# Kernel optimization log

Measured on AMD Instinct MI355X. Metric: run time of the kernel, lower is better.

## Reference

```python
import jax, jax.numpy as jnp
import numpy as np

B = 2
IM_H, IM_W = 240, 320
ENV_ROW, ENV_COL = 120, 160
ENV_H, ENV_W = 8, 16
GRID = 8
NGRIDS = 6 * GRID * GRID  # 384
BASIS = [(3, 2, 0), (7, 6, 4), (4, 5, 0), (6, 2, 5), (7, 6, 3), (7, 3, 4)]
# extra_transform_matrix @ extra_transform_matrix_LightNet, applied to row vectors
M12 = jnp.asarray(np.array([[0., 0., 1.], [0., -1., 0.], [1., 0., 0.]], np.float32)
                  @ np.array([[1., 0., 0.], [0., -1., 0.], [0., 0., -1.]], np.float32))


def _normalize(v, axis):
    return v / jnp.maximum(jnp.linalg.norm(v, axis=axis, keepdims=True), 1e-12)


def _inv3x3(A):
    # closed-form adjugate inverse of batched 3x3 (replaces torch.inverse)
    a, b, c = A[..., 0, 0], A[..., 0, 1], A[..., 0, 2]
    d, e, f = A[..., 1, 0], A[..., 1, 1], A[..., 1, 2]
    g, h, i = A[..., 2, 0], A[..., 2, 1], A[..., 2, 2]
    c00 = e * i - f * h; c01 = f * g - d * i; c02 = d * h - e * g
    c10 = c * h - b * i; c11 = a * i - c * g; c12 = b * g - a * h
    c20 = b * f - c * e; c21 = c * d - a * f; c22 = a * e - b * d
    det = a * c00 + b * c01 + c * c02
    inv = jnp.stack([jnp.stack([c00, c10, c20], -1),
                     jnp.stack([c01, c11, c21], -1),
                     jnp.stack([c02, c12, c22], -1)], -2)
    return inv / det[..., None, None]


def _camera_frame(normalPred):
    # renderingLayer.forwardEnv(if_normal_only=True): pool normal to env res,
    # renormalize, build per-pixel (camx, camy, normal) frame with up=[0,1,0]
    r = IM_H // ENV_ROW
    n = normalPred.reshape(normalPred.shape[0], 3, ENV_ROW, r, ENV_COL, r).mean(axis=(3, 5))
    n = n / jnp.sqrt(jnp.clip(jnp.sum(n * n, axis=1, keepdims=True), 1e-6, 1.0))
    up = jnp.array([0., 1., 0.], n.dtype).reshape(1, 3, 1, 1)
    camy = _normalize(up - jnp.sum(up * n, axis=1, keepdims=True) * n, 1)
    camx = -_normalize(jnp.cross(camy, n, axis=1), 1)
    return camx, camy, n


def _grid_centers(layout, cam_R):
    # get_grid_centers: 6 walls x GRID x GRID cell centers, transformed to LightNet frame.
    # The transform is linear with t=0, so mean-of-4-corners == center = b1*(i+.5)+b2*(j+.5)+o.
    o = jnp.stack([layout[:, t[0]] for t in BASIS], 1)                 # (B,6,3)
    b1 = (jnp.stack([layout[:, t[1]] for t in BASIS], 1) - o) / GRID
    b2 = (jnp.stack([layout[:, t[2]] for t in BASIS], 1) - o) / GRID
    ii, jj = jnp.meshgrid(jnp.arange(GRID, dtype=layout.dtype), jnp.arange(GRID, dtype=layout.dtype), indexing='ij')
    ctr = (b1[:, :, None, None, :] * (ii + 0.5)[None, None, :, :, None]
           + b2[:, :, None, None, :] * (jj + 0.5)[None, None, :, :, None]
           + o[:, :, None, None, :])                                   # (B,6,G,G,3)
    ctr = jnp.einsum('bji,bfghj->bfghi', cam_R, ctr)                   # R^T @ v
    ctr = jnp.einsum('bfghi,ij->bfghj', ctr, M12)                      # row-vec @ M1 @ M2
    return ctr.reshape(layout.shape[0], -1, 3)                         # (B, 384, 3)


def _sample_env_border(env, x, y):
    # grid_sample(align_corners=True, padding_mode='border') on the 8x16 env hemisphere.
    # With align_corners=True the normalized uv unnormalizes back to pixel coords (az, el).
    H, W = ENV_H, ENV_W
    x = jnp.clip(x, 0.0, W - 1.0); y = jnp.clip(y, 0.0, H - 1.0)
    x0f = jnp.floor(x); y0f = jnp.floor(y)
    wx = (x - x0f)[..., None]; wy = (y - y0f)[..., None]
    x0 = x0f.astype(jnp.int32); y0 = y0f.astype(jnp.int32)
    x1 = jnp.minimum(x0 + 1, W - 1); y1 = jnp.minimum(y0 + 1, H - 1)
    envp = jnp.transpose(env, (0, 1, 2, 4, 5, 3)).reshape(env.shape[0], ENV_ROW, ENV_COL, H * W, 3)

    def g(yy, xx):
        return jnp.take_along_axis(envp, (yy * W + xx)[..., None], axis=3)  # (B,R,C,N,3)

    return (g(y0, x0) * (1 - wy) * (1 - wx) + g(y0, x1) * (1 - wy) * wx
            + g(y1, x0) * wy * (1 - wx) + g(y1, x1) * wy * wx)


def _forward(normalPred, depthPred, envmapsPredImage, cam_K, cam_R, layout):
    f_pix = (cam_K[:, 0, 0] * (IM_W / 2.0) / cam_K[:, 0, 2])[:, None, None]
    vv, uu = jnp.meshgrid(jnp.arange(IM_H, dtype=depthPred.dtype), jnp.arange(IM_W, dtype=depthPred.dtype), indexing='ij')
    z = -depthPred
    points = jnp.stack([-(uu - IM_W / 2.0) / f_pix * z, (vv - IM_H / 2.0) / f_pix * z, z], axis=1)  # (B,3,IM_H,IM_W)

    camx, camy, nrm = _camera_frame(normalPred)      # (B,3,R,C) each
    centers = _grid_centers(layout, cam_R)           # (B,NG,3)

    r = IM_H // ENV_ROW
    pts = jnp.transpose(points[:, :, ::r, ::r], (0, 2, 3, 1))  # (B,R,C,3)
    mask = (pts[..., 2] < -0.1).astype(points.dtype)           # (B,R,C)

    A = jnp.stack([jnp.transpose(camx, (0, 2, 3, 1)),
                   jnp.transpose(camy, (0, 2, 3, 1)),
                   jnp.transpose(nrm, (0, 2, 3, 1))], axis=-1)  # (B,R,C,3,3) columns
    Ainv = _inv3x3(A + 1e-6 * jnp.eye(3, dtype=A.dtype))

    vec = centers[:, :, None, None, :] - pts[:, None]           # (B,NG,R,C,3)
    l = jnp.einsum('brcij,bnrcj->bnrci', Ainv, vec)
    l = l / jnp.linalg.norm(l, axis=-1, keepdims=True)
    cos_t = jnp.clip(l[..., 2], -1.0, 1.0)
    theta = jnp.arccos(cos_t)
    sin_t = jnp.sin(theta)
    phi = jnp.arctan2(l[..., 1] / sin_t, l[..., 0] / sin_t)
    az = (phi / (2.0 * np.pi) + 0.5) * ENV_W - 0.5              # (B,NG,R,C)
    el = theta / np.pi * 2.0 * ENV_H - 0.5

    env = jnp.transpose(envmapsPredImage, (0, 2, 3, 1, 4, 5))   # (B,R,C,3,H,W)
    sampled = _sample_env_border(env, jnp.transpose(az, (0, 2, 3, 1)), jnp.transpose(el, (0, 2, 3, 1)))  # (B,R,C,NG,3)

    acc = jnp.transpose(sampled, (0, 4, 3, 1, 2)) * mask[:, None, None] * 0.1  # (B,3,NG,R,C)
    mask_exp = mask[:, None, None]                                             # (B,1,1,R,C)
    mean = jnp.transpose(acc.sum((-1, -2)) / (mask_exp.sum((-1, -2)) + 1e-6), (0, 2, 1))  # (B,NG,3)
    return acc, mask_exp, mean


def setup_inputs() -> dict:
    key = jax.random.key(0)
    k1, k2, k3, k4, k5, k6 = jax.random.split(key, 6)
    normalPred = jax.random.normal(k1, (B, 3, IM_H, IM_W), jnp.float32)
    normalPred = normalPred / jnp.maximum(jnp.linalg.norm(normalPred, axis=1, keepdims=True), 1e-6)
    depthPred = jax.random.uniform(k2, (B, IM_H, IM_W), jnp.float32, 0.5, 5.5)
    envmapsPredImage = jax.random.uniform(k3, (B, 3, ENV_ROW, ENV_COL, ENV_H, ENV_W), jnp.float32)
    f = 250.0 + 100.0 * jax.random.uniform(k4, (B,), jnp.float32)
    z0 = jnp.zeros((B,), jnp.float32); o1 = jnp.ones((B,), jnp.float32)
    cam_K = jnp.stack([jnp.stack([f, z0, o1 * (IM_W / 2.0)], -1),
                       jnp.stack([z0, f, o1 * (IM_H / 2.0)], -1),
                       jnp.stack([z0, z0, o1], -1)], 1)
    ang = jax.random.uniform(k5, (B,), jnp.float32, -0.3, 0.3)
    ca, sa = jnp.cos(ang), jnp.sin(ang)
    cam_R = jnp.stack([jnp.stack([ca, z0, sa], -1),
                       jnp.stack([z0, o1, z0], -1),
                       jnp.stack([-sa, z0, ca], -1)], 1)
    box = jnp.asarray(np.array([[-3, -1.5, -3], [3, -1.5, -3], [3, -1.5, 3], [-3, -1.5, 3],
                                [-3, 1.5, -3], [3, 1.5, -3], [3, 1.5, 3], [-3, 1.5, 3]], np.float32))
    layout = box[None] + 0.05 * jax.random.normal(k6, (B, 8, 3), jnp.float32)
    return {"normalPred": normalPred, "depthPred": depthPred, "envmapsPredImage": envmapsPredImage,
            "cam_K": cam_K, "cam_R": cam_R, "layout": layout}


def reference(normalPred, depthPred, envmapsPredImage, cam_K, cam_R, layout):
    # returns (envmap_lightAccu, points_sampled_mask_expanded, envmap_lightAccu_mean)
    return _forward(normalPred, depthPred, envmapsPredImage, cam_K, cam_R, layout)
```

## Files before the change

kernel.cpp:

```cpp
#include <hip/hip_runtime.h>

typedef unsigned short u16;
typedef unsigned int   u32;

#define IM_H    240
#define IM_W    320
#define ENV_COL 160
#define NPIX    19200
#define NGRIDS  384
#define BATCH   2

#define ACC_SIZE (BATCH*3*NGRIDS*NPIX)
#define MASK_OFF ACC_SIZE
#define MEAN_OFF (ACC_SIZE + BATCH*NPIX)

#define NREP    8
#define WS_SUM8    0
#define WS_MSUM8   (BATCH*NREP*1152)
#define WS_ZERO_F  (WS_MSUM8 + BATCH*NREP)

#define PI_F  3.14159265358979f
#define PI_2F 1.57079632679490f

__device__ __forceinline__ u16 f2bf(float f) {
    u32 x = __float_as_uint(f);
    x += 0x7fffu + ((x >> 16) & 1u);
    return (u16)(x >> 16);
}

__device__ __forceinline__ float row16_sum(float v) {
    v += __int_as_float(__builtin_amdgcn_update_dpp(
             0, __float_as_int(v), 0x128, 0xf, 0xf, false));
    v += __int_as_float(__builtin_amdgcn_update_dpp(
             0, __float_as_int(v), 0x124, 0xf, 0xf, false));
    v += __int_as_float(__builtin_amdgcn_update_dpp(
             0, __float_as_int(v), 0x122, 0xf, 0xf, false));
    v += __int_as_float(__builtin_amdgcn_update_dpp(
             0, __float_as_int(v), 0x121, 0xf, 0xf, false));
    return v;
}

__device__ __forceinline__ float fast_acos(float x) {
    float ax = fabsf(x);
    float s  = sqrtf(fmaxf(1.0f - ax, 0.0f));
    float p  = ((-0.0187293f * ax + 0.0742610f) * ax - 0.2121144f) * ax + 1.5707288f;
    float r  = s * p;
    return (x < 0.0f) ? (PI_F - r) : r;
}

__device__ __forceinline__ float fast_atan2(float y, float x) {
    float ax = fabsf(x), ay = fabsf(y);
    float mx = fmaxf(ax, ay), mn = fminf(ax, ay);
    float t  = mn * __builtin_amdgcn_rcpf(fmaxf(mx, 1e-37f));
    float t2 = t * t;
    float p  = ((((0.0208351f * t2 - 0.0851330f) * t2 + 0.1801410f) * t2
                 - 0.3302995f) * t2 + 0.9998660f) * t;
    p = (ay > ax) ? (PI_2F - p) : p;
    p = (x < 0.0f) ? (PI_F - p) : p;
    return __builtin_copysignf(p, y);
}

__global__ __launch_bounds__(256, 4) void k_main(
        const float* __restrict__ normal,
        const float* __restrict__ depth,
        const float* __restrict__ envm,
        const float* __restrict__ camK,
        const float* __restrict__ camR,
        const float* __restrict__ layout,
        float* __restrict__ wsum8,
        float* __restrict__ msum8,
        float* __restrict__ out) {

    __shared__ __align__(16) u32   env01[128 * 32];
    __shared__               u16   env2 [128 * 32];
    __shared__ __align__(16) float cen_s[NGRIDS * 4];
    __shared__               float pgeo[32][13];
    __shared__               float psum[NGRIDS * 3];
    __shared__               float pmask;

    const int tid = threadIdx.x;
    const int bid = blockIdx.x;
    const int b   = bid / 600;
    const int pg  = bid % 600;
    const int p0  = pg * 32;

    for (int i = tid; i < NGRIDS * 3; i += 256) psum[i] = 0.0f;
    if (tid == 0) pmask = 0.0f;

    {
        const int B0[6] = {3, 7, 4, 6, 7, 7};
        const int B1[6] = {2, 6, 5, 2, 6, 3};
        const int B2[6] = {0, 4, 0, 5, 3, 4};
        for (int idx = tid; idx < NGRIDS; idx += 256) {
            int f = idx >> 6, gi = (idx >> 3) & 7, hj = idx & 7;
            int t0 = B0[f], t1 = B1[f], t2 = B2[f];
            float cw[3];
            #pragma unroll
            for (int j = 0; j < 3; ++j) {
                float o  = layout[(b * 8 + t0) * 3 + j];
                float e1 = (layout[(b * 8 + t1) * 3 + j] - o) * 0.125f;
                float e2 = (layout[(b * 8 + t2) * 3 + j] - o) * 0.125f;
                cw[j] = e1 * ((float)gi + 0.5f) + e2 * ((float)hj + 0.5f) + o;
            }
            float v0 = camR[b*9+0]*cw[0] + camR[b*9+3]*cw[1] + camR[b*9+6]*cw[2];
            float v1 = camR[b*9+1]*cw[0] + camR[b*9+4]*cw[1] + camR[b*9+7]*cw[2];
            float v2 = camR[b*9+2]*cw[0] + camR[b*9+5]*cw[1] + camR[b*9+8]*cw[2];
            cen_s[idx * 4 + 0] = v2;
            cen_s[idx * 4 + 1] = v1;
            cen_s[idx * 4 + 2] = -v0;
            cen_s[idx * 4 + 3] = 0.0f;
        }
    }

    #pragma unroll
    for (int k = 0; k < 4; ++k) {
        int ci  = tid + k * 256;
        int pix = ci & 31;
        int tq  = ci >> 5;
        size_t base = ((size_t)b * 3 * NPIX + p0 + pix) * 128 + tq * 4;
        const float4 v0 = *reinterpret_cast<const float4*>(&envm[base]);
        const float4 v1 = *reinterpret_cast<const float4*>(&envm[base + (size_t)NPIX * 128]);
        const float4 v2 = *reinterpret_cast<const float4*>(&envm[base + (size_t)2 * NPIX * 128]);
        const float a0[4] = {v0.x, v0.y, v0.z, v0.w};
        const float a1[4] = {v1.x, v1.y, v1.z, v1.w};
        const float a2[4] = {v2.x, v2.y, v2.z, v2.w};
        #pragma unroll
        for (int j = 0; j < 4; ++j) {
            int t = tq * 4 + j;
            env01[t * 32 + pix] = ((u32)f2bf(a1[j]) << 16) | (u32)f2bf(a0[j]);
            env2 [t * 32 + pix] = f2bf(a2[j]);
        }
    }

    if (tid < 32) {
        int p = p0 + tid;
        int r = p / ENV_COL, c = p % ENV_COL;
        float nv[3];
        #pragma unroll
        for (int ch = 0; ch < 3; ++ch) {
            const float* np_ = &normal[((size_t)(b * 3 + ch) * IM_H + 2 * r) * IM_W + 2 * c];
            nv[ch] = 0.25f * (np_[0] + np_[1] + np_[IM_W] + np_[IM_W + 1]);
        }
        float s2 = nv[0]*nv[0] + nv[1]*nv[1] + nv[2]*nv[2];
        s2 = fminf(fmaxf(s2, 1e-6f), 1.0f);
        float inv = 1.0f / sqrtf(s2);
        nv[0] *= inv; nv[1] *= inv; nv[2] *= inv;
        float ty0 = -nv[1]*nv[0], ty1 = 1.0f - nv[1]*nv[1], ty2 = -nv[1]*nv[2];
        float tn = fmaxf(sqrtf(ty0*ty0 + ty1*ty1 + ty2*ty2), 1e-12f);
        float cy0 = ty0/tn, cy1 = ty1/tn, cy2 = ty2/tn;
        float cr0 = cy1*nv[2] - cy2*nv[1];
        float cr1 = cy2*nv[0] - cy0*nv[2];
        float cr2 = cy0*nv[1] - cy1*nv[0];
        float cnm = fmaxf(sqrtf(cr0*cr0 + cr1*cr1 + cr2*cr2), 1e-12f);
        float cx0 = -cr0/cnm, cx1 = -cr1/cnm, cx2 = -cr2/cnm;
        float a = cx0 + 1e-6f, bb = cy0,         cc = nv[0];
        float d = cx1,         e  = cy1 + 1e-6f, f  = nv[1];
        float g2 = cx2,        h  = cy2,         i  = nv[2] + 1e-6f;
        float c00 = e*i - f*h,   c01 = f*g2 - d*i,  c02 = d*h - e*g2;
        float c10 = cc*h - bb*i, c11 = a*i - cc*g2, c12 = bb*g2 - a*h;
        float c20 = bb*f - cc*e, c21 = cc*d - a*f,  c22 = a*e - bb*d;
        float rdet = 1.0f / (a*c00 + bb*c01 + cc*c02);
        float K00 = camK[b * 9 + 0];
        float K02 = camK[b * 9 + 2];
        float fpix = K00 * (IM_W / 2.0f) / K02;
        float z = -depth[((size_t)b * IM_H + 2 * r) * IM_W + 2 * c];
        float px = -((2.0f * c) - IM_W / 2.0f) / fpix * z;
        float py =  ((2.0f * r) - IM_H / 2.0f) / fpix * z;
        float mask = (z < -0.1f) ? 1.0f : 0.0f;
        pgeo[tid][0] = px;  pgeo[tid][1] = py;  pgeo[tid][2] = z;
        pgeo[tid][3] = c00*rdet; pgeo[tid][4]  = c10*rdet; pgeo[tid][5]  = c20*rdet;
        pgeo[tid][6] = c01*rdet; pgeo[tid][7]  = c11*rdet; pgeo[tid][8]  = c21*rdet;
        pgeo[tid][9] = c02*rdet; pgeo[tid][10] = c12*rdet; pgeo[tid][11] = c22*rdet;
        pgeo[tid][12] = mask;
        out[MASK_OFF + (size_t)b * NPIX + p] = mask;
    }

    __syncthreads();

    if (tid < 32) {
        float ms = row16_sum(pgeo[tid][12]);
        if ((tid & 15) == 0) atomicAdd(&pmask, ms);
    }

    const int pix  = tid & 31;
    const int slot = tid >> 5;
    const float ptx = pgeo[pix][0], pty = pgeo[pix][1], ptz = pgeo[pix][2];
    const float A0 = pgeo[pix][3], A1 = pgeo[pix][4],  A2 = pgeo[pix][5];
    const float A3 = pgeo[pix][6], A4 = pgeo[pix][7],  A5 = pgeo[pix][8];
    const float A6 = pgeo[pix][9], A7 = pgeo[pix][10], A8 = pgeo[pix][11];
    const float mscale = pgeo[pix][12] * 0.1f;

    #pragma unroll 4
    for (int it = 0; it < 48; ++it) {
        const int n = it * 8 + slot;
        const float4 cc4 = *reinterpret_cast<const float4*>(&cen_s[n * 4]);
        const float vx = cc4.x - ptx;
        const float vy = cc4.y - pty;
        const float vz = cc4.z - ptz;
        float lx = A0 * vx + A1 * vy + A2 * vz;
        float ly = A3 * vx + A4 * vy + A5 * vz;
        float lz = A6 * vx + A7 * vy + A8 * vz;
        float rn = __builtin_amdgcn_rsqf(lx * lx + ly * ly + lz * lz);
        float ct = fminf(fmaxf(lz * rn, -1.0f), 1.0f);
        float theta = fast_acos(ct);
        float phi = fast_atan2(ly, lx);
        float az = phi * 2.54647908947032537f + 7.5f;
        float el = theta * 5.09295817894065074f - 0.5f;
        float x = fminf(fmaxf(az, 0.0f), 15.0f);
        float y = fminf(fmaxf(el, 0.0f), 7.0f);
        float x0f = floorf(x), y0f = floorf(y);
        float wx = x - x0f, wy = y - y0f;
        int ix0 = (int)x0f, iy0 = (int)y0f;
        int ix1 = min(ix0 + 1, 15), iy1 = min(iy0 + 1, 7);
        int t00 = (iy0 << 4) + ix0;
        int t01 = (iy0 << 4) + ix1;
        int t10 = (iy1 << 4) + ix0;
        int t11 = (iy1 << 4) + ix1;
        u32 c00 = env01[(t00 << 5) + pix], c01 = env01[(t01 << 5) + pix];
        u32 c10 = env01[(t10 << 5) + pix], c11 = env01[(t11 << 5) + pix];
        u32 g00 = env2 [(t00 << 5) + pix], g01 = env2 [(t01 << 5) + pix];
        u32 g10 = env2 [(t10 << 5) + pix], g11 = env2 [(t11 << 5) + pix];
        float wy1m = wy * mscale, wy0m = mscale - wy1m;
        float w00 = wy0m * (1.0f - wx), w01 = wy0m * wx;
        float w10 = wy1m * (1.0f - wx), w11 = wy1m * wx;
        float v0 = w00 * __uint_as_float(c00 << 16)
                 + w01 * __uint_as_float(c01 << 16)
                 + w10 * __uint_as_float(c10 << 16)
                 + w11 * __uint_as_float(c11 << 16);
        float v1 = w00 * __uint_as_float(c00 & 0xffff0000u)
                 + w01 * __uint_as_float(c01 & 0xffff0000u)
                 + w10 * __uint_as_float(c10 & 0xffff0000u)
                 + w11 * __uint_as_float(c11 & 0xffff0000u);
        float v2 = w00 * __uint_as_float(g00 << 16)
                 + w01 * __uint_as_float(g01 << 16)
                 + w10 * __uint_as_float(g10 << 16)
                 + w11 * __uint_as_float(g11 << 16);

        size_t obase = ((size_t)b * 3 * NGRIDS + n) * NPIX + p0 + pix;
        out[obase]                             = v0;
        out[obase + (size_t)NGRIDS * NPIX]     = v1;
        out[obase + (size_t)2 * NGRIDS * NPIX] = v2;

        float s0 = row16_sum(v0);
        float s1 = row16_sum(v1);
        float s2v = row16_sum(v2);
        if ((pix & 15) == 0) {
            atomicAdd(&psum[n * 3 + 0], s0);
            atomicAdd(&psum[n * 3 + 1], s1);
            atomicAdd(&psum[n * 3 + 2], s2v);
        }
    }

    __syncthreads();
    {
        float* wrep = &wsum8[((size_t)b * NREP + (bid & (NREP - 1))) * (NGRIDS * 3)];
        for (int i = tid; i < NGRIDS * 3; i += 256)
            atomicAdd(&wrep[i], psum[i]);
        if (tid == 0)
            atomicAdd(&msum8[b * NREP + (bid & (NREP - 1))], pmask);
    }
}

__global__ __launch_bounds__(256) void k_final(const float* __restrict__ wsum8,
                                               const float* __restrict__ msum8,
                                               float* __restrict__ out) {
    int t = blockIdx.x * 256 + threadIdx.x;
    if (t >= BATCH * NGRIDS * 3) return;
    int b = t / (NGRIDS * 3);
    int i = t % (NGRIDS * 3);
    float ms = 0.0f;
    #pragma unroll
    for (int r = 0; r < NREP; ++r) ms += msum8[b * NREP + r];
    float s = 0.0f;
    #pragma unroll
    for (int r = 0; r < NREP; ++r)
        s += wsum8[((size_t)b * NREP + r) * (NGRIDS * 3) + i];
    out[MEAN_OFF + t] = s / (ms + 1e-6f);
}

extern "C" void kernel_launch(void* const* d_in, const int* in_sizes, int n_in,
                              void* d_out, int out_size, void* d_ws, size_t ws_size,
                              hipStream_t stream) {
    const float* normal = (const float*)d_in[0];
    const float* depth  = (const float*)d_in[1];
    const float* envm   = (const float*)d_in[2];
    const float* camK   = (const float*)d_in[3];
    const float* camR   = (const float*)d_in[4];
    const float* layout = (const float*)d_in[5];
    float* out = (float*)d_out;
    float* ws  = (float*)d_ws;

    hipMemsetAsync(ws, 0, WS_ZERO_F * sizeof(float), stream);
    k_main<<<dim3(BATCH * 600), dim3(256), 0, stream>>>(normal, depth, envm, camK,
                                                        camR, layout,
                                                        ws + WS_SUM8, ws + WS_MSUM8,
                                                        out);
    k_final<<<dim3(9), dim3(256), 0, stream>>>(ws + WS_SUM8, ws + WS_MSUM8, out);
}
```

Measured before the change: 274.5 us.

## Replace atomic reductions with per-block partial sums and a two-stage final reduce

Each block now writes its half-wave partial sums of the envmap values and of the mask directly to a workspace buffer instead of doing shared-memory atomics followed by global atomics into replicated accumulators. The memset of the workspace is removed. The final kernel becomes a tree reduction over 1200 partials per output element. This removes the atomic contention and the memset launch, but adds roughly 10 MB of partial-sum writes and a strided gather read in k_final.

```diff
diff --git a/kernel.cpp b/kernel.cpp
--- a/kernel.cpp
+++ b/kernel.cpp
@@ -14,10 +14,9 @@
 #define MASK_OFF ACC_SIZE
 #define MEAN_OFF (ACC_SIZE + BATCH*NPIX)
 
-#define NREP    8
-#define WS_SUM8    0
-#define WS_MSUM8   (BATCH*NREP*1152)
-#define WS_ZERO_F  (WS_MSUM8 + BATCH*NREP)
+#define WS_WPART   0
+#define WPART_N    (BATCH*600*2*1152)
+#define WS_MPART   WPART_N
 
 #define PI_F  3.14159265358979f
 #define PI_2F 1.57079632679490f
@@ -67,25 +66,20 @@
         const float* __restrict__ camK,
         const float* __restrict__ camR,
         const float* __restrict__ layout,
-        float* __restrict__ wsum8,
-        float* __restrict__ msum8,
+        float* __restrict__ wpart,
+        float* __restrict__ mpart,
         float* __restrict__ out) {
 
     __shared__ __align__(16) u32   env01[128 * 32];
     __shared__               u16   env2 [128 * 32];
     __shared__ __align__(16) float cen_s[NGRIDS * 4];
     __shared__               float pgeo[32][13];
-    __shared__               float psum[NGRIDS * 3];
-    __shared__               float pmask;
 
     const int tid = threadIdx.x;
     const int bid = blockIdx.x;
     const int b   = bid / 600;
     const int pg  = bid % 600;
     const int p0  = pg * 32;
-
-    for (int i = tid; i < NGRIDS * 3; i += 256) psum[i] = 0.0f;
-    if (tid == 0) pmask = 0.0f;
 
     {
         const int B0[6] = {3, 7, 4, 6, 7, 7};
@@ -173,14 +167,11 @@
         pgeo[tid][9] = c02*rdet; pgeo[tid][10] = c12*rdet; pgeo[tid][11] = c22*rdet;
         pgeo[tid][12] = mask;
         out[MASK_OFF + (size_t)b * NPIX + p] = mask;
+        float ms = row16_sum(mask);
+        if ((tid & 15) == 0) mpart[bid * 2 + (tid >> 4)] = ms;
     }
 
     __syncthreads();
-
-    if (tid < 32) {
-        float ms = row16_sum(pgeo[tid][12]);
-        if ((tid & 15) == 0) atomicAdd(&pmask, ms);
-    }
 
     const int pix  = tid & 31;
     const int slot = tid >> 5;
@@ -189,6 +180,7 @@
     const float A3 = pgeo[pix][6], A4 = pgeo[pix][7],  A5 = pgeo[pix][8];
     const float A6 = pgeo[pix][9], A7 = pgeo[pix][10], A8 = pgeo[pix][11];
     const float mscale = pgeo[pix][12] * 0.1f;
+    float* const wbase = &wpart[((size_t)bid * 2 + (pix >> 4)) * 1152];
 
     #pragma unroll 4
     for (int it = 0; it < 48; ++it) {
@@ -245,37 +237,36 @@
         float s1 = row16_sum(v1);
         float s2v = row16_sum(v2);
         if ((pix & 15) == 0) {
-            atomicAdd(&psum[n * 3 + 0], s0);
-            atomicAdd(&psum[n * 3 + 1], s1);
-            atomicAdd(&psum[n * 3 + 2], s2v);
-        }
-    }
-
+            float* wp = wbase + n * 3;
+            wp[0] = s0;
+            wp[1] = s1;
+            wp[2] = s2v;
+        }
+    }
+}
+
+__global__ __launch_bounds__(256) void k_final(const float* __restrict__ wpart,
+                                               const float* __restrict__ mpart,
+                                               float* __restrict__ out) {
+    const int bid = blockIdx.x;
+    const int tid = threadIdx.x;
+    const int b   = bid / 1152;
+    const int i   = bid % 1152;
+    float s = 0.0f, ms = 0.0f;
+    for (int j = tid; j < 1200; j += 256) {
+        s  += wpart[((size_t)b * 1200 + j) * 1152 + i];
+        ms += mpart[b * 1200 + j];
+    }
+    __shared__ float r1[256], r2[256];
+    r1[tid] = s; r2[tid] = ms;
     __syncthreads();
-    {
-        float* wrep = &wsum8[((size_t)b * NREP + (bid & (NREP - 1))) * (NGRIDS * 3)];
-        for (int i = tid; i < NGRIDS * 3; i += 256)
-            atomicAdd(&wrep[i], psum[i]);
-        if (tid == 0)
-            atomicAdd(&msum8[b * NREP + (bid & (NREP - 1))], pmask);
-    }
-}
-
-__global__ __launch_bounds__(256) void k_final(const float* __restrict__ wsum8,
-                                               const float* __restrict__ msum8,
-                                               float* __restrict__ out) {
-    int t = blockIdx.x * 256 + threadIdx.x;
-    if (t >= BATCH * NGRIDS * 3) return;
-    int b = t / (NGRIDS * 3);
-    int i = t % (NGRIDS * 3);
-    float ms = 0.0f;
     #pragma unroll
-    for (int r = 0; r < NREP; ++r) ms += msum8[b * NREP + r];
-    float s = 0.0f;
-    #pragma unroll
-    for (int r = 0; r < NREP; ++r)
-        s += wsum8[((size_t)b * NREP + r) * (NGRIDS * 3) + i];
-    out[MEAN_OFF + t] = s / (ms + 1e-6f);
+    for (int m = 128; m >= 1; m >>= 1) {
+        if (tid < m) { r1[tid] += r1[tid + m]; r2[tid] += r2[tid + m]; }
+        __syncthreads();
+    }
+    if (tid == 0)
+        out[MEAN_OFF + bid] = r1[0] / (r2[0] + 1e-6f);
 }
 
 extern "C" void kernel_launch(void* const* d_in, const int* in_sizes, int n_in,
@@ -290,10 +281,10 @@
     float* out = (float*)d_out;
     float* ws  = (float*)d_ws;
 
-    hipMemsetAsync(ws, 0, WS_ZERO_F * sizeof(float), stream);
     k_main<<<dim3(BATCH * 600), dim3(256), 0, stream>>>(normal, depth, envm, camK,
                                                         camR, layout,
-                                                        ws + WS_SUM8, ws + WS_MSUM8,
+                                                        ws + WS_WPART, ws + WS_MPART,
                                                         out);
-    k_final<<<dim3(9), dim3(256), 0, stream>>>(ws + WS_SUM8, ws + WS_MSUM8, out);
-}
+    k_final<<<dim3(BATCH * 1152), dim3(256), 0, stream>>>(ws + WS_WPART,
+                                                          ws + WS_MPART, out);
+}
```

Result: slower. 295.2 us (+7.5%).

## Precompute grid centers in separate kernel and compute pixel geometry per-thread

Applied to the files above, without the earlier changes.

Moves the grid-center computation out of k_main into a tiny k_centers kernel that writes centers to workspace; k_main then reads them from global memory (L1/L2 cached) instead of shared memory. Per-pixel geometry is now computed redundantly by all 256 threads in registers rather than by 32 threads and shared via LDS. Together these free shared memory (cen_s, pgeo) and raise launch_bounds occupancy target from 4 to 5 blocks per SM. The trade-off is an extra launch, 8x redundant per-pixel geometry and normal loads, and global-memory center loads in the hot loop.

```diff
diff --git a/kernel.cpp b/kernel.cpp
--- a/kernel.cpp
+++ b/kernel.cpp
@@ -18,6 +18,7 @@
 #define WS_SUM8    0
 #define WS_MSUM8   (BATCH*NREP*1152)
 #define WS_ZERO_F  (WS_MSUM8 + BATCH*NREP)
+#define WS_CEN     WS_ZERO_F
 
 #define PI_F  3.14159265358979f
 #define PI_2F 1.57079632679490f
@@ -60,21 +61,46 @@
     return __builtin_copysignf(p, y);
 }
 
-__global__ __launch_bounds__(256, 4) void k_main(
+__global__ __launch_bounds__(256) void k_centers(const float* __restrict__ layout,
+                                                 const float* __restrict__ camR,
+                                                 float* __restrict__ cen) {
+    int t = blockIdx.x * 256 + threadIdx.x;
+    if (t >= BATCH * NGRIDS) return;
+    int b = t / NGRIDS, n = t % NGRIDS;
+    int f = n >> 6, gi = (n >> 3) & 7, hj = n & 7;
+    const int B0[6] = {3, 7, 4, 6, 7, 7};
+    const int B1[6] = {2, 6, 5, 2, 6, 3};
+    const int B2[6] = {0, 4, 0, 5, 3, 4};
+    int t0 = B0[f], t1 = B1[f], t2 = B2[f];
+    float cw[3];
+    #pragma unroll
+    for (int j = 0; j < 3; ++j) {
+        float o  = layout[(b * 8 + t0) * 3 + j];
+        float e1 = (layout[(b * 8 + t1) * 3 + j] - o) * 0.125f;
+        float e2 = (layout[(b * 8 + t2) * 3 + j] - o) * 0.125f;
+        cw[j] = e1 * ((float)gi + 0.5f) + e2 * ((float)hj + 0.5f) + o;
+    }
+    float v0 = camR[b*9+0]*cw[0] + camR[b*9+3]*cw[1] + camR[b*9+6]*cw[2];
+    float v1 = camR[b*9+1]*cw[0] + camR[b*9+4]*cw[1] + camR[b*9+7]*cw[2];
+    float v2 = camR[b*9+2]*cw[0] + camR[b*9+5]*cw[1] + camR[b*9+8]*cw[2];
+    cen[t * 4 + 0] = v2;
+    cen[t * 4 + 1] = v1;
+    cen[t * 4 + 2] = -v0;
+    cen[t * 4 + 3] = 0.0f;
+}
+
+__global__ __launch_bounds__(256, 5) void k_main(
         const float* __restrict__ normal,
         const float* __restrict__ depth,
         const float* __restrict__ envm,
         const float* __restrict__ camK,
-        const float* __restrict__ camR,
-        const float* __restrict__ layout,
+        const float* __restrict__ cen,
         float* __restrict__ wsum8,
         float* __restrict__ msum8,
         float* __restrict__ out) {
 
     __shared__ __align__(16) u32   env01[128 * 32];
     __shared__               u16   env2 [128 * 32];
-    __shared__ __align__(16) float cen_s[NGRIDS * 4];
-    __shared__               float pgeo[32][13];
     __shared__               float psum[NGRIDS * 3];
     __shared__               float pmask;
 
@@ -83,41 +109,18 @@
     const int b   = bid / 600;
     const int pg  = bid % 600;
     const int p0  = pg * 32;
+    const int pix  = tid & 31;
+    const int slot = tid >> 5;
 
     for (int i = tid; i < NGRIDS * 3; i += 256) psum[i] = 0.0f;
     if (tid == 0) pmask = 0.0f;
 
-    {
-        const int B0[6] = {3, 7, 4, 6, 7, 7};
-        const int B1[6] = {2, 6, 5, 2, 6, 3};
-        const int B2[6] = {0, 4, 0, 5, 3, 4};
-        for (int idx = tid; idx < NGRIDS; idx += 256) {
-            int f = idx >> 6, gi = (idx >> 3) & 7, hj = idx & 7;
-            int t0 = B0[f], t1 = B1[f], t2 = B2[f];
-            float cw[3];
-            #pragma unroll
-            for (int j = 0; j < 3; ++j) {
-                float o  = layout[(b * 8 + t0) * 3 + j];
-                float e1 = (layout[(b * 8 + t1) * 3 + j] - o) * 0.125f;
-                float e2 = (layout[(b * 8 + t2) * 3 + j] - o) * 0.125f;
-                cw[j] = e1 * ((float)gi + 0.5f) + e2 * ((float)hj + 0.5f) + o;
-            }
-            float v0 = camR[b*9+0]*cw[0] + camR[b*9+3]*cw[1] + camR[b*9+6]*cw[2];
-            float v1 = camR[b*9+1]*cw[0] + camR[b*9+4]*cw[1] + camR[b*9+7]*cw[2];
-            float v2 = camR[b*9+2]*cw[0] + camR[b*9+5]*cw[1] + camR[b*9+8]*cw[2];
-            cen_s[idx * 4 + 0] = v2;
-            cen_s[idx * 4 + 1] = v1;
-            cen_s[idx * 4 + 2] = -v0;
-            cen_s[idx * 4 + 3] = 0.0f;
-        }
-    }
-
     #pragma unroll
     for (int k = 0; k < 4; ++k) {
         int ci  = tid + k * 256;
-        int pix = ci & 31;
+        int px_ = ci & 31;
         int tq  = ci >> 5;
-        size_t base = ((size_t)b * 3 * NPIX + p0 + pix) * 128 + tq * 4;
+        size_t base = ((size_t)b * 3 * NPIX + p0 + px_) * 128 + tq * 4;
         const float4 v0 = *reinterpret_cast<const float4*>(&envm[base]);
         const float4 v1 = *reinterpret_cast<const float4*>(&envm[base + (size_t)NPIX * 128]);
         const float4 v2 = *reinterpret_cast<const float4*>(&envm[base + (size_t)2 * NPIX * 128]);
@@ -127,13 +130,14 @@
         #pragma unroll
         for (int j = 0; j < 4; ++j) {
             int t = tq * 4 + j;
-            env01[t * 32 + pix] = ((u32)f2bf(a1[j]) << 16) | (u32)f2bf(a0[j]);
-            env2 [t * 32 + pix] = f2bf(a2[j]);
+            env01[t * 32 + px_] = ((u32)f2bf(a1[j]) << 16) | (u32)f2bf(a0[j]);
+            env2 [t * 32 + px_] = f2bf(a2[j]);
         }
     }
 
-    if (tid < 32) {
-        int p = p0 + tid;
+    float ptx, pty, ptz, A0, A1, A2, A3, A4, A5, A6, A7, A8, mask;
+    {
+        int p = p0 + pix;
         int r = p / ENV_COL, c = p % ENV_COL;
         float nv[3];
         #pragma unroll
@@ -164,36 +168,30 @@
         float K02 = camK[b * 9 + 2];
         float fpix = K00 * (IM_W / 2.0f) / K02;
         float z = -depth[((size_t)b * IM_H + 2 * r) * IM_W + 2 * c];
-        float px = -((2.0f * c) - IM_W / 2.0f) / fpix * z;
-        float py =  ((2.0f * r) - IM_H / 2.0f) / fpix * z;
-        float mask = (z < -0.1f) ? 1.0f : 0.0f;
-        pgeo[tid][0] = px;  pgeo[tid][1] = py;  pgeo[tid][2] = z;
-        pgeo[tid][3] = c00*rdet; pgeo[tid][4]  = c10*rdet; pgeo[tid][5]  = c20*rdet;
-        pgeo[tid][6] = c01*rdet; pgeo[tid][7]  = c11*rdet; pgeo[tid][8]  = c21*rdet;
-        pgeo[tid][9] = c02*rdet; pgeo[tid][10] = c12*rdet; pgeo[tid][11] = c22*rdet;
-        pgeo[tid][12] = mask;
-        out[MASK_OFF + (size_t)b * NPIX + p] = mask;
+        ptx = -((2.0f * c) - IM_W / 2.0f) / fpix * z;
+        pty =  ((2.0f * r) - IM_H / 2.0f) / fpix * z;
+        ptz = z;
+        mask = (z < -0.1f) ? 1.0f : 0.0f;
+        A0 = c00*rdet; A1 = c10*rdet; A2 = c20*rdet;
+        A3 = c01*rdet; A4 = c11*rdet; A5 = c21*rdet;
+        A6 = c02*rdet; A7 = c12*rdet; A8 = c22*rdet;
+        if (tid < 32) out[MASK_OFF + (size_t)b * NPIX + p] = mask;
     }
 
     __syncthreads();
 
     if (tid < 32) {
-        float ms = row16_sum(pgeo[tid][12]);
+        float ms = row16_sum(mask);
         if ((tid & 15) == 0) atomicAdd(&pmask, ms);
     }
 
-    const int pix  = tid & 31;
-    const int slot = tid >> 5;
-    const float ptx = pgeo[pix][0], pty = pgeo[pix][1], ptz = pgeo[pix][2];
-    const float A0 = pgeo[pix][3], A1 = pgeo[pix][4],  A2 = pgeo[pix][5];
-    const float A3 = pgeo[pix][6], A4 = pgeo[pix][7],  A5 = pgeo[pix][8];
-    const float A6 = pgeo[pix][9], A7 = pgeo[pix][10], A8 = pgeo[pix][11];
-    const float mscale = pgeo[pix][12] * 0.1f;
+    const float mscale = mask * 0.1f;
+    const float* const cbase = &cen[(size_t)b * NGRIDS * 4];
 
     #pragma unroll 4
     for (int it = 0; it < 48; ++it) {
         const int n = it * 8 + slot;
-        const float4 cc4 = *reinterpret_cast<const float4*>(&cen_s[n * 4]);
+        const float4 cc4 = *reinterpret_cast<const float4*>(&cbase[n * 4]);
         const float vx = cc4.x - ptx;
         const float vy = cc4.y - pty;
         const float vz = cc4.z - ptz;
@@ -291,8 +289,9 @@
     float* ws  = (float*)d_ws;
 
     hipMemsetAsync(ws, 0, WS_ZERO_F * sizeof(float), stream);
+    k_centers<<<dim3(3), dim3(256), 0, stream>>>(layout, camR, ws + WS_CEN);
     k_main<<<dim3(BATCH * 600), dim3(256), 0, stream>>>(normal, depth, envm, camK,
-                                                        camR, layout,
+                                                        ws + WS_CEN,
                                                         ws + WS_SUM8, ws + WS_MSUM8,
                                                         out);
     k_final<<<dim3(9), dim3(256), 0, stream>>>(ws + WS_SUM8, ws + WS_MSUM8, out);
```

After: 273.1 us. Within noise of the previous version (-0.5%).
